# Optimization experiments

Measured on AMD Instinct MI355X. Metric: run time of the kernel, lower is better.

## Reference

```python
import jax
import jax.numpy as jnp
import numpy as np

TIME_DIVISION = 2
FILL_DIST = 50000.0  # sentinel initial distance, as in the torch module


def setup_inputs() -> dict:
    key = jax.random.key(0)
    k1, k2 = jax.random.split(key)
    B, T, H, W, C = 4, 16, 28, 28, 35
    TT = T // TIME_DIVISION
    x = jax.random.normal(k1, (B, T, H, W, C), dtype=jnp.float32)
    init_ = jax.random.randint(k2, (B * TIME_DIVISION,), 0, TT * H * W, dtype=jnp.int64)
    return {"x": x, "init_": init_, "k": 256}


def _pairwise_dist(xf):
    # xf: (Bt, N, C) -> (Bt, N, N) euclidean distances (torch.cdist p=2)
    sq = jnp.sum(xf * xf, axis=-1)                      # (Bt, N)
    gram = jnp.einsum('bnc,bmc->bnm', xf, xf)           # (Bt, N, N)
    d2 = jnp.maximum(sq[:, :, None] + sq[:, None, :] - 2.0 * gram, 0.0)
    return jnp.sqrt(d2)


def reference(x, init_, k):
    B, T, H, W, C = x.shape
    TT = T // TIME_DIVISION
    N = TT * H * W                 # points per time segment
    Bt = B * TIME_DIVISION
    k_ = k // TIME_DIVISION

    xf = x.reshape(Bt, N, C)
    cdist = _pairwise_dist(xf)
    # set diagonal to -1 (self-distance excluded from argmax)
    diag = jnp.arange(N)
    cdist = cdist.at[:, diag, diag].set(-1.0)

    b_idx = jnp.arange(Bt)
    farthest0 = jnp.remainder(init_, N)
    distance0 = jnp.full((Bt, N), FILL_DIST, dtype=x.dtype)

    def step(carry, _):
        distance, farthest = carry
        dist = cdist[b_idx, farthest]                   # (Bt, N) gather rows
        distance = jnp.minimum(dist, distance)
        farthest = jnp.argmax(distance, axis=-1)
        return (distance, farthest), farthest

    _, rest = jax.lax.scan(step, (distance0, farthest0), None, length=k_ - 1)
    sampling_index = jnp.concatenate([farthest0[None], rest], axis=0).T  # (Bt, k_)

    # add per-time-segment index offsets, flatten to (B, td*k_)
    offsets = (jnp.arange(TIME_DIVISION) * (TT * H * W))[None, :, None]
    sampling_index = sampling_index.reshape(B, TIME_DIVISION, k_) + offsets
    sampling_index = sampling_index.reshape(B, TIME_DIVISION * k_)

    # gather feature channels (first C-3; last 3 are positional encodings)
    xflat = x.reshape(B, T * H * W, C)
    patches = xflat[jnp.arange(B)[:, None], sampling_index][:, :, : C - 3]
    return patches, sampling_index
```

## Files before the change

kernel.cpp:

```cpp
#include <hip/hip_runtime.h>


#define NPTS 6272
#define CDIM 35
#define BT   8
#define KSEL 128
#define THW  12544
#define BPS  16
#define PPB  392
#define BLK  256
#define NB   (BT * BPS)
#define TAILN (PPB - BLK)

__device__ __forceinline__ unsigned long long key_of(float v, int j) {
  unsigned int u = __float_as_uint(v);
  u = (u & 0x80000000u) ? ~u : (u | 0x80000000u);
  return ((unsigned long long)u << 32) | (unsigned int)(NPTS - j);
}
__device__ __forceinline__ unsigned long long kmax(unsigned long long a,
                                                   unsigned long long b) {
  return a > b ? a : b;
}
__device__ __forceinline__ unsigned long long merge64(unsigned long long a,
                                                      unsigned long long t) {
  unsigned int lo = (unsigned int)a > (unsigned int)t ? (unsigned int)a : (unsigned int)t;
  unsigned int ah = (unsigned int)(a >> 32), th = (unsigned int)(t >> 32);
  unsigned int hi = ah > th ? ah : th;
  return ((unsigned long long)hi << 32) | lo;
}

template <int CTRL, int RMASK, bool BC>
__device__ __forceinline__ unsigned long long dpp_kmax(unsigned long long k) {
  unsigned int lo = (unsigned int)k, hi = (unsigned int)(k >> 32);
  unsigned int tlo = (unsigned int)__builtin_amdgcn_update_dpp(0, (int)lo, CTRL, RMASK, 0xF, BC);
  unsigned int thi = (unsigned int)__builtin_amdgcn_update_dpp(0, (int)hi, CTRL, RMASK, 0xF, BC);
  unsigned long long t = ((unsigned long long)thi << 32) | tlo;
  return kmax(k, t);
}
__device__ __forceinline__ unsigned long long wave_kmax64(unsigned long long k) {
  k = dpp_kmax<0x111, 0xF, true >(k);
  k = dpp_kmax<0x112, 0xF, true >(k);
  k = dpp_kmax<0x114, 0xF, true >(k);
  k = dpp_kmax<0x118, 0xF, true >(k);
  k = dpp_kmax<0x142, 0xA, false>(k);
  k = dpp_kmax<0x143, 0xC, false>(k);
  unsigned int rlo = (unsigned int)__builtin_amdgcn_readlane((int)(unsigned int)k, 63);
  unsigned int rhi = (unsigned int)__builtin_amdgcn_readlane((int)(k >> 32), 63);
  return ((unsigned long long)rhi << 32) | rlo;
}
__device__ __forceinline__ unsigned long long row16_kmax(unsigned long long k) {
  k = dpp_kmax<0x111, 0xF, true>(k);
  k = dpp_kmax<0x112, 0xF, true>(k);
  k = dpp_kmax<0x114, 0xF, true>(k);
  k = dpp_kmax<0x118, 0xF, true>(k);
  unsigned int rlo = (unsigned int)__builtin_amdgcn_readlane((int)(unsigned int)k, 15);
  unsigned int rhi = (unsigned int)__builtin_amdgcn_readlane((int)(k >> 32), 15);
  return ((unsigned long long)rhi << 32) | rlo;
}

__device__ __forceinline__ unsigned long long load_l2(const unsigned long long* p) {
  unsigned long long r;
  asm volatile("global_load_dwordx2 %0, %1, off sc0\n\ts_waitcnt vmcnt(0)"
               : "=&v"(r) : "v"(p) : "memory");
  return r;
}
__device__ __forceinline__ unsigned long long load_llc(const unsigned long long* p) {
  unsigned long long r;
  asm volatile("global_load_dwordx2 %0, %1, off sc0 sc1\n\ts_waitcnt vmcnt(0)"
               : "=&v"(r) : "v"(p) : "memory");
  return r;
}
__device__ __forceinline__ void store_plain(unsigned long long* p, unsigned long long v) {
  asm volatile("global_store_dwordx2 %0, %1, off" :: "v"(p), "v"(v) : "memory");
}

__global__ __attribute__((amdgpu_waves_per_eu(1, 1))) __launch_bounds__(BLK)
void fps_kernel(const float* __restrict__ x,
                const int* __restrict__ init_,
                float* __restrict__ patches,
                float* __restrict__ sidx,
                unsigned long long* __restrict__ slots,
                unsigned long long* __restrict__ probe) {
  __shared__ unsigned long long wk[4];
  __shared__ int far_s;

  const int bid  = (int)blockIdx.x;
  const int b    = bid & 7;
  const int sub  = bid >> 3;
  const int tid  = (int)threadIdx.x;
  const int lane = tid & 63;
  const int wid  = tid >> 6;
  const int j0   = sub * PPB;
  const int td   = b & 1;
  const float* xg = x + (size_t)b * NPTS * CDIM;
  unsigned long long* seg = slots + (size_t)b * KSEL * BPS;
  unsigned long long* prb = probe + (size_t)b * KSEL * BPS;

  if (tid >= 1 && tid < KSEL)
    store_plain(&prb[tid * BPS + sub], 0ull);

  float xr0[CDIM], xr1[CDIM];
  float sqr0, sqr1, df0, df1;
  {
    const float* src0 = xg + (size_t)(j0 + tid) * CDIM;
    float acc = 0.0f;
    {
#pragma clang fp contract(off)
#pragma unroll
      for (int c = 0; c < CDIM; ++c) { float v = src0[c]; xr0[c] = v; acc = acc + v * v; }
    }
    sqr0 = acc; df0 = 50000.0f;
    sqr1 = 0.0f; df1 = 50000.0f;
#pragma unroll
    for (int c = 0; c < CDIM; ++c) xr1[c] = 0.0f;
    if (tid < TAILN) {
      const float* src1 = xg + (size_t)(j0 + BLK + tid) * CDIM;
      float acc1 = 0.0f;
      {
#pragma clang fp contract(off)
#pragma unroll
        for (int c = 0; c < CDIM; ++c) { float v = src1[c]; xr1[c] = v; acc1 = acc1 + v * v; }
      }
      sqr1 = acc1;
    }
#pragma unroll
    for (int c = 0; c < CDIM; ++c) {
      asm volatile("" : "+v"(xr0[c]));
      asm volatile("" : "+v"(xr1[c]));
    }
    asm volatile("" : "+v"(sqr0));
    asm volatile("" : "+v"(sqr1));
  }

  asm volatile("s_waitcnt vmcnt(0)" ::: "memory");
  if (tid == 0)
    __hip_atomic_store(&seg[sub], 1ull, __ATOMIC_RELAXED, __HIP_MEMORY_SCOPE_AGENT);
  if (tid < BPS) {
    while (__hip_atomic_load(&seg[tid], __ATOMIC_RELAXED,
                             __HIP_MEMORY_SCOPE_AGENT) == 0ull) {}
  }
  __syncthreads();

  int far;
  { int f = init_[b] % NPTS; if (f < 0) f += NPTS; far = f; }
  if (sub == 0) {
    if (tid == 0) sidx[b * KSEL] = (float)(far + td * NPTS);
    if (tid < 32) patches[(size_t)(b * KSEL) * 32 + tid] = xg[(size_t)far * CDIM + tid];
  }

  for (int step = 1; step < KSEL; ++step) {
    const int fu = __builtin_amdgcn_readfirstlane(far);
    const float* fx = xg + (size_t)fu * CDIM;
    float xf[CDIM];
#pragma unroll
    for (int c = 0; c < CDIM; ++c) xf[c] = fx[c];

    float sqf;
    {
#pragma clang fp contract(off)
      float a = 0.0f;
#pragma unroll
      for (int c = 0; c < CDIM; ++c) { float t = xf[c]; a = a + t * t; }
      sqf = a;
    }

    unsigned long long bk;
    {
      float dot = 0.0f;
#pragma unroll
      for (int c = 0; c < CDIM; ++c)
        dot = __builtin_fmaf(xf[c], xr0[c], dot);
      float d2;
      {
#pragma clang fp contract(off)
        d2 = (sqf + sqr0) - 2.0f * dot;
      }
      d2 = fmaxf(d2, 0.0f);
      float d = __fsqrt_rn(d2);
      const int j = j0 + tid;
      d = (j == far) ? -1.0f : d;
      float nd = fminf(d, df0);
      df0 = nd;
      bk = key_of(nd, j);
    }
    if (tid < TAILN) {
      float dot = 0.0f;
#pragma unroll
      for (int c = 0; c < CDIM; ++c)
        dot = __builtin_fmaf(xf[c], xr1[c], dot);
      float d2;
      {
#pragma clang fp contract(off)
        d2 = (sqf + sqr1) - 2.0f * dot;
      }
      d2 = fmaxf(d2, 0.0f);
      float d = __fsqrt_rn(d2);
      const int j = j0 + BLK + tid;
      d = (j == far) ? -1.0f : d;
      float nd = fminf(d, df1);
      df1 = nd;
      bk = kmax(bk, key_of(nd, j));
    }

    bk = wave_kmax64(bk);
    if (lane == 0) wk[wid] = bk;
    __syncthreads();

    if (tid < BPS) {
      if (tid == 0) {
        unsigned long long m = kmax(kmax(wk[0], wk[1]), kmax(wk[2], wk[3]));
        store_plain(&prb[step * BPS + sub], m);
        __hip_atomic_store(&seg[step * BPS + sub], m,
                           __ATOMIC_RELAXED, __HIP_MEMORY_SCOPE_AGENT);
      }
      asm volatile("" ::: "memory");
      unsigned long long k = 0ull;
      const unsigned long long* pp = &prb[step * BPS + tid];
      const unsigned long long* sp = &seg[step * BPS + tid];
      while (__any(k == 0ull)) {
#pragma unroll
        for (int q = 0; q < 3; ++q) {
          if (__any(k == 0ull)) {
            if (k == 0ull) k = merge64(k, load_l2(pp));
            __builtin_amdgcn_s_sleep(1);
          }
        }
        if (k == 0ull) k = merge64(k, load_llc(sp));
      }
      k = row16_kmax(k);
      if (tid == 0)
        far_s = NPTS - (int)(unsigned int)(k & 0xFFFFFFFFull);
    }
    __syncthreads();
    far = far_s;

    if (sub == 0) {
      if (tid == 0) sidx[b * KSEL + step] = (float)(far + td * NPTS);
      if (tid < 32) patches[(size_t)(b * KSEL + step) * 32 + tid] =
                        xg[(size_t)far * CDIM + tid];
    }
  }
}

extern "C" void kernel_launch(void* const* d_in, const int* in_sizes, int n_in,
                              void* d_out, int out_size, void* d_ws, size_t ws_size,
                              hipStream_t stream) {
  const float* x    = (const float*)d_in[0];
  const int*   init = (const int*)d_in[1];
  (void)in_sizes; (void)n_in; (void)out_size; (void)ws_size;

  const size_t arr = (size_t)BT * KSEL * BPS * sizeof(unsigned long long);
  unsigned long long* slots = (unsigned long long*)d_ws;
  unsigned long long* probe = (unsigned long long*)((char*)d_ws + arr);

  float* patches = (float*)d_out;
  float* sidx    = patches + (size_t)4 * 256 * 32;

  hipMemsetAsync(d_ws, 0, 2 * arr, stream);

  void* kargs[] = { (void*)&x, (void*)&init, (void*)&patches, (void*)&sidx,
                    (void*)&slots, (void*)&probe };
  hipLaunchCooperativeKernel((const void*)fps_kernel, dim3(NB), dim3(BLK),
                             kargs, 0, stream);
}
```

Measured before the change: 218.5 us.

## Poll cross-block slots via scalar loads in every wave, drop post-poll barrier

Each wave now polls the 16 per-block partial maxima for the step itself, using a burst of scalar s_load_dwordx2 after s_dcache_inv. This replaces having 16 threads poll with vector loads and then broadcast through shared memory behind a second __syncthreads. If scalar polling fails twice the kernel falls back to LLC vector loads. The aim is to cut barrier and broadcast latency in the serial 127-step chain. The cost is more polling traffic from four waves per block, and correctness now depends on scalar-cache invalidation seeing the stored values.

```diff
diff --git a/kernel.cpp b/kernel.cpp
--- a/kernel.cpp
+++ b/kernel.cpp
@@ -58,12 +58,6 @@
   return ((unsigned long long)rhi << 32) | rlo;
 }
 
-__device__ __forceinline__ unsigned long long load_l2(const unsigned long long* p) {
-  unsigned long long r;
-  asm volatile("global_load_dwordx2 %0, %1, off sc0\n\ts_waitcnt vmcnt(0)"
-               : "=&v"(r) : "v"(p) : "memory");
-  return r;
-}
 __device__ __forceinline__ unsigned long long load_llc(const unsigned long long* p) {
   unsigned long long r;
   asm volatile("global_load_dwordx2 %0, %1, off sc0 sc1\n\ts_waitcnt vmcnt(0)"
@@ -82,7 +76,6 @@
                 unsigned long long* __restrict__ slots,
                 unsigned long long* __restrict__ probe) {
   __shared__ unsigned long long wk[4];
-  __shared__ int far_s;
 
   const int bid  = (int)blockIdx.x;
   const int b    = bid & 7;
@@ -143,10 +136,12 @@
 
   int far;
   { int f = init_[b] % NPTS; if (f < 0) f += NPTS; far = f; }
-  if (sub == 0) {
-    if (tid == 0) sidx[b * KSEL] = (float)(far + td * NPTS);
-    if (tid < 32) patches[(size_t)(b * KSEL) * 32 + tid] = xg[(size_t)far * CDIM + tid];
+  if (sub == 0 && wid == 0) {
+    if (lane == 0) sidx[b * KSEL] = (float)(far + td * NPTS);
+    if (lane < 32) patches[(size_t)(b * KSEL) * 32 + lane] = xg[(size_t)far * CDIM + lane];
   }
+
+  int cap = 8, fails = 0;
 
   for (int step = 1; step < KSEL; ++step) {
     const int fu = __builtin_amdgcn_readfirstlane(far);
@@ -206,38 +201,85 @@
     if (lane == 0) wk[wid] = bk;
     __syncthreads();
 
-    if (tid < BPS) {
-      if (tid == 0) {
-        unsigned long long m = kmax(kmax(wk[0], wk[1]), kmax(wk[2], wk[3]));
-        store_plain(&prb[step * BPS + sub], m);
-        __hip_atomic_store(&seg[step * BPS + sub], m,
-                           __ATOMIC_RELAXED, __HIP_MEMORY_SCOPE_AGENT);
-      }
-      asm volatile("" ::: "memory");
-      unsigned long long k = 0ull;
-      const unsigned long long* pp = &prb[step * BPS + tid];
-      const unsigned long long* sp = &seg[step * BPS + tid];
+    if (tid == 0) {
+      unsigned long long m = kmax(kmax(wk[0], wk[1]), kmax(wk[2], wk[3]));
+      store_plain(&prb[step * BPS + sub], m);
+      __hip_atomic_store(&seg[step * BPS + sub], m,
+                         __ATOMIC_RELAXED, __HIP_MEMORY_SCOPE_AGENT);
+    }
+    asm volatile("" ::: "memory");
+
+    bool got = false;
+    if (cap > 0) {
+      const unsigned long long* srow = prb + (size_t)step * BPS;
+      for (int it = 0; it < cap && !got; ++it) {
+        unsigned long long k0,k1,k2,k3,k4,k5,k6,k7,k8,k9,k10,k11,k12,k13,k14,k15;
+        asm volatile(
+            "s_dcache_inv\n\t"
+            "s_load_dwordx2 %[a0],  %[bp], 0x0\n\t"
+            "s_load_dwordx2 %[a1],  %[bp], 0x8\n\t"
+            "s_load_dwordx2 %[a2],  %[bp], 0x10\n\t"
+            "s_load_dwordx2 %[a3],  %[bp], 0x18\n\t"
+            "s_load_dwordx2 %[a4],  %[bp], 0x20\n\t"
+            "s_load_dwordx2 %[a5],  %[bp], 0x28\n\t"
+            "s_load_dwordx2 %[a6],  %[bp], 0x30\n\t"
+            "s_load_dwordx2 %[a7],  %[bp], 0x38\n\t"
+            "s_load_dwordx2 %[a8],  %[bp], 0x40\n\t"
+            "s_load_dwordx2 %[a9],  %[bp], 0x48\n\t"
+            "s_load_dwordx2 %[a10], %[bp], 0x50\n\t"
+            "s_load_dwordx2 %[a11], %[bp], 0x58\n\t"
+            "s_load_dwordx2 %[a12], %[bp], 0x60\n\t"
+            "s_load_dwordx2 %[a13], %[bp], 0x68\n\t"
+            "s_load_dwordx2 %[a14], %[bp], 0x70\n\t"
+            "s_load_dwordx2 %[a15], %[bp], 0x78\n\t"
+            "s_waitcnt lgkmcnt(0)"
+            : [a0]"=s"(k0),  [a1]"=s"(k1),  [a2]"=s"(k2),  [a3]"=s"(k3),
+              [a4]"=s"(k4),  [a5]"=s"(k5),  [a6]"=s"(k6),  [a7]"=s"(k7),
+              [a8]"=s"(k8),  [a9]"=s"(k9),  [a10]"=s"(k10),[a11]"=s"(k11),
+              [a12]"=s"(k12),[a13]"=s"(k13),[a14]"=s"(k14),[a15]"=s"(k15)
+            : [bp]"s"(srow)
+            : "memory");
+        unsigned int mn = (unsigned int)k0;
+        mn = mn < (unsigned int)k1  ? mn : (unsigned int)k1;
+        mn = mn < (unsigned int)k2  ? mn : (unsigned int)k2;
+        mn = mn < (unsigned int)k3  ? mn : (unsigned int)k3;
+        mn = mn < (unsigned int)k4  ? mn : (unsigned int)k4;
+        mn = mn < (unsigned int)k5  ? mn : (unsigned int)k5;
+        mn = mn < (unsigned int)k6  ? mn : (unsigned int)k6;
+        mn = mn < (unsigned int)k7  ? mn : (unsigned int)k7;
+        mn = mn < (unsigned int)k8  ? mn : (unsigned int)k8;
+        mn = mn < (unsigned int)k9  ? mn : (unsigned int)k9;
+        mn = mn < (unsigned int)k10 ? mn : (unsigned int)k10;
+        mn = mn < (unsigned int)k11 ? mn : (unsigned int)k11;
+        mn = mn < (unsigned int)k12 ? mn : (unsigned int)k12;
+        mn = mn < (unsigned int)k13 ? mn : (unsigned int)k13;
+        mn = mn < (unsigned int)k14 ? mn : (unsigned int)k14;
+        mn = mn < (unsigned int)k15 ? mn : (unsigned int)k15;
+        if (mn != 0u) {
+          unsigned long long mx = kmax(kmax(kmax(k0, k1), kmax(k2, k3)),
+                                       kmax(kmax(k4, k5), kmax(k6, k7)));
+          mx = kmax(mx, kmax(kmax(kmax(k8, k9), kmax(k10, k11)),
+                             kmax(kmax(k12, k13), kmax(k14, k15))));
+          far = NPTS - (int)(unsigned int)(mx & 0xFFFFFFFFull);
+          got = true;
+        }
+      }
+      if (!got && ++fails >= 2) cap = 0;
+    }
+    if (!got) {
+      unsigned long long k = (lane < BPS) ? 0ull : ~0ull;
+      const unsigned long long* sp = &seg[(size_t)step * BPS + (lane & 15)];
       while (__any(k == 0ull)) {
-#pragma unroll
-        for (int q = 0; q < 3; ++q) {
-          if (__any(k == 0ull)) {
-            if (k == 0ull) k = merge64(k, load_l2(pp));
-            __builtin_amdgcn_s_sleep(1);
-          }
-        }
         if (k == 0ull) k = merge64(k, load_llc(sp));
       }
       k = row16_kmax(k);
-      if (tid == 0)
-        far_s = NPTS - (int)(unsigned int)(k & 0xFFFFFFFFull);
-    }
-    __syncthreads();
-    far = far_s;
-
-    if (sub == 0) {
-      if (tid == 0) sidx[b * KSEL + step] = (float)(far + td * NPTS);
-      if (tid < 32) patches[(size_t)(b * KSEL + step) * 32 + tid] =
-                        xg[(size_t)far * CDIM + tid];
+      far = NPTS - (int)(unsigned int)(k & 0xFFFFFFFFull);
+    }
+
+    if (sub == 0 && wid == 0) {
+      if (lane == 0) sidx[b * KSEL + step] = (float)(far + td * NPTS);
+      if (lane < 32) patches[(size_t)(b * KSEL + step) * 32 + lane] =
+                         xg[(size_t)far * CDIM + lane];
     }
   }
 }
```

After: 232.0 us. 6.2% more time.

## Replace block-level sync with per-wave global slot exchange for argmax reduction

Applied to the files above, without the earlier changes.

Each wave now publishes its own argmax key to a 64-slot global array per step, and every wave independently polls all 64 slots and reduces them with a wave-wide DPP max. This removes the two __syncthreads per step, the shared-memory staging, the separate probe array with its L2-then-LLC polling, and the initial grid barrier. It trades these for four times as many global stores and every wave polling with LLC loads, which may add memory traffic and contention while shortening the critical path of each step.

```diff
diff --git a/kernel.cpp b/kernel.cpp
--- a/kernel.cpp
+++ b/kernel.cpp
@@ -11,6 +11,7 @@
 #define BLK  256
 #define NB   (BT * BPS)
 #define TAILN (PPB - BLK)
+#define SPS  64
 
 __device__ __forceinline__ unsigned long long key_of(float v, int j) {
   unsigned int u = __float_as_uint(v);
@@ -20,13 +21,6 @@
 __device__ __forceinline__ unsigned long long kmax(unsigned long long a,
                                                    unsigned long long b) {
   return a > b ? a : b;
-}
-__device__ __forceinline__ unsigned long long merge64(unsigned long long a,
-                                                      unsigned long long t) {
-  unsigned int lo = (unsigned int)a > (unsigned int)t ? (unsigned int)a : (unsigned int)t;
-  unsigned int ah = (unsigned int)(a >> 32), th = (unsigned int)(t >> 32);
-  unsigned int hi = ah > th ? ah : th;
-  return ((unsigned long long)hi << 32) | lo;
 }
 
 template <int CTRL, int RMASK, bool BC>
@@ -48,42 +42,20 @@
   unsigned int rhi = (unsigned int)__builtin_amdgcn_readlane((int)(k >> 32), 63);
   return ((unsigned long long)rhi << 32) | rlo;
 }
-__device__ __forceinline__ unsigned long long row16_kmax(unsigned long long k) {
-  k = dpp_kmax<0x111, 0xF, true>(k);
-  k = dpp_kmax<0x112, 0xF, true>(k);
-  k = dpp_kmax<0x114, 0xF, true>(k);
-  k = dpp_kmax<0x118, 0xF, true>(k);
-  unsigned int rlo = (unsigned int)__builtin_amdgcn_readlane((int)(unsigned int)k, 15);
-  unsigned int rhi = (unsigned int)__builtin_amdgcn_readlane((int)(k >> 32), 15);
-  return ((unsigned long long)rhi << 32) | rlo;
-}
-
-__device__ __forceinline__ unsigned long long load_l2(const unsigned long long* p) {
-  unsigned long long r;
-  asm volatile("global_load_dwordx2 %0, %1, off sc0\n\ts_waitcnt vmcnt(0)"
-               : "=&v"(r) : "v"(p) : "memory");
-  return r;
-}
+
 __device__ __forceinline__ unsigned long long load_llc(const unsigned long long* p) {
   unsigned long long r;
   asm volatile("global_load_dwordx2 %0, %1, off sc0 sc1\n\ts_waitcnt vmcnt(0)"
                : "=&v"(r) : "v"(p) : "memory");
   return r;
 }
-__device__ __forceinline__ void store_plain(unsigned long long* p, unsigned long long v) {
-  asm volatile("global_store_dwordx2 %0, %1, off" :: "v"(p), "v"(v) : "memory");
-}
 
 __global__ __attribute__((amdgpu_waves_per_eu(1, 1))) __launch_bounds__(BLK)
 void fps_kernel(const float* __restrict__ x,
                 const int* __restrict__ init_,
                 float* __restrict__ patches,
                 float* __restrict__ sidx,
-                unsigned long long* __restrict__ slots,
-                unsigned long long* __restrict__ probe) {
-  __shared__ unsigned long long wk[4];
-  __shared__ int far_s;
-
+                unsigned long long* __restrict__ slots) {
   const int bid  = (int)blockIdx.x;
   const int b    = bid & 7;
   const int sub  = bid >> 3;
@@ -93,11 +65,7 @@
   const int j0   = sub * PPB;
   const int td   = b & 1;
   const float* xg = x + (size_t)b * NPTS * CDIM;
-  unsigned long long* seg = slots + (size_t)b * KSEL * BPS;
-  unsigned long long* prb = probe + (size_t)b * KSEL * BPS;
-
-  if (tid >= 1 && tid < KSEL)
-    store_plain(&prb[tid * BPS + sub], 0ull);
+  unsigned long long* seg = slots + (size_t)b * KSEL * SPS;
 
   float xr0[CDIM], xr1[CDIM];
   float sqr0, sqr1, df0, df1;
@@ -132,20 +100,11 @@
     asm volatile("" : "+v"(sqr1));
   }
 
-  asm volatile("s_waitcnt vmcnt(0)" ::: "memory");
-  if (tid == 0)
-    __hip_atomic_store(&seg[sub], 1ull, __ATOMIC_RELAXED, __HIP_MEMORY_SCOPE_AGENT);
-  if (tid < BPS) {
-    while (__hip_atomic_load(&seg[tid], __ATOMIC_RELAXED,
-                             __HIP_MEMORY_SCOPE_AGENT) == 0ull) {}
-  }
-  __syncthreads();
-
   int far;
   { int f = init_[b] % NPTS; if (f < 0) f += NPTS; far = f; }
-  if (sub == 0) {
-    if (tid == 0) sidx[b * KSEL] = (float)(far + td * NPTS);
-    if (tid < 32) patches[(size_t)(b * KSEL) * 32 + tid] = xg[(size_t)far * CDIM + tid];
+  if (sub == 0 && wid == 0) {
+    if (lane == 0) sidx[b * KSEL] = (float)(far + td * NPTS);
+    if (lane < 32) patches[(size_t)(b * KSEL) * 32 + lane] = xg[(size_t)far * CDIM + lane];
   }
 
   for (int step = 1; step < KSEL; ++step) {
@@ -203,41 +162,23 @@
     }
 
     bk = wave_kmax64(bk);
-    if (lane == 0) wk[wid] = bk;
-    __syncthreads();
-
-    if (tid < BPS) {
-      if (tid == 0) {
-        unsigned long long m = kmax(kmax(wk[0], wk[1]), kmax(wk[2], wk[3]));
-        store_plain(&prb[step * BPS + sub], m);
-        __hip_atomic_store(&seg[step * BPS + sub], m,
-                           __ATOMIC_RELAXED, __HIP_MEMORY_SCOPE_AGENT);
-      }
-      asm volatile("" ::: "memory");
-      unsigned long long k = 0ull;
-      const unsigned long long* pp = &prb[step * BPS + tid];
-      const unsigned long long* sp = &seg[step * BPS + tid];
-      while (__any(k == 0ull)) {
-#pragma unroll
-        for (int q = 0; q < 3; ++q) {
-          if (__any(k == 0ull)) {
-            if (k == 0ull) k = merge64(k, load_l2(pp));
-            __builtin_amdgcn_s_sleep(1);
-          }
-        }
-        if (k == 0ull) k = merge64(k, load_llc(sp));
-      }
-      k = row16_kmax(k);
-      if (tid == 0)
-        far_s = NPTS - (int)(unsigned int)(k & 0xFFFFFFFFull);
-    }
-    __syncthreads();
-    far = far_s;
-
-    if (sub == 0) {
-      if (tid == 0) sidx[b * KSEL + step] = (float)(far + td * NPTS);
-      if (tid < 32) patches[(size_t)(b * KSEL + step) * 32 + tid] =
-                        xg[(size_t)far * CDIM + tid];
+    if (lane == 0)
+      __hip_atomic_store(&seg[(size_t)step * SPS + sub * 4 + wid], bk,
+                         __ATOMIC_RELAXED, __HIP_MEMORY_SCOPE_AGENT);
+    asm volatile("" ::: "memory");
+
+    unsigned long long k = 0ull;
+    const unsigned long long* sp = &seg[(size_t)step * SPS + lane];
+    while (__any(k == 0ull)) {
+      if (k == 0ull) k = load_llc(sp);
+    }
+    k = wave_kmax64(k);
+    far = NPTS - (int)(unsigned int)(k & 0xFFFFFFFFull);
+
+    if (sub == 0 && wid == 0) {
+      if (lane == 0) sidx[b * KSEL + step] = (float)(far + td * NPTS);
+      if (lane < 32) patches[(size_t)(b * KSEL + step) * 32 + lane] =
+                         xg[(size_t)far * CDIM + lane];
     }
   }
 }
@@ -249,17 +190,16 @@
   const int*   init = (const int*)d_in[1];
   (void)in_sizes; (void)n_in; (void)out_size; (void)ws_size;
 
-  const size_t arr = (size_t)BT * KSEL * BPS * sizeof(unsigned long long);
   unsigned long long* slots = (unsigned long long*)d_ws;
-  unsigned long long* probe = (unsigned long long*)((char*)d_ws + arr);
+  const size_t slots_bytes = (size_t)BT * KSEL * SPS * sizeof(unsigned long long);
 
   float* patches = (float*)d_out;
   float* sidx    = patches + (size_t)4 * 256 * 32;
 
-  hipMemsetAsync(d_ws, 0, 2 * arr, stream);
+  hipMemsetAsync(d_ws, 0, slots_bytes, stream);
 
   void* kargs[] = { (void*)&x, (void*)&init, (void*)&patches, (void*)&sidx,
-                    (void*)&slots, (void*)&probe };
+                    (void*)&slots };
   hipLaunchCooperativeKernel((const void*)fps_kernel, dim3(NB), dim3(BLK),
                              kargs, 0, stream);
 }
```

Result: slower. 453.5 us (+107.6%).
